# Optimization experiments

Measured on AMD Instinct MI355X. Metric: run time of the kernel, lower is better.

The kernel has to match this reference:

```python
import jax, jax.numpy as jnp
import numpy as np

B, N, E, C, M = 4, 16384, 65536, 256, 64

def setup_inputs() -> dict:
    key = jax.random.key(0)
    ks = jax.random.split(key, 12)
    s = 1.0 / np.sqrt(C)
    return {
        'x': jax.random.normal(ks[0], (B, N, C), jnp.float32),
        'edge_attr': jax.random.normal(ks[1], (B, E, 1), jnp.float32),
        'edge_idx': jax.random.randint(ks[2], (B, E, 2), 0, N, jnp.int32),
        'W_fx': jax.random.normal(ks[3], (C, C), jnp.float32) * s,
        'b_fx': jnp.zeros((C,), jnp.float32),
        'W_x': jax.random.normal(ks[4], (C, C), jnp.float32) * s,
        'b_x': jnp.zeros((C,), jnp.float32),
        'W_slice': jax.random.normal(ks[5], (C, M), jnp.float32) * s,
        'b_slice': jnp.zeros((M,), jnp.float32),
        'temp_x': jnp.full((1, 1, M), 0.5, jnp.float32),
        'ph_x': jax.random.uniform(ks[6], (1, 1, C), jnp.float32) / C,
        'W_fedge': jax.random.normal(ks[7], (1, C), jnp.float32),
        'b_fedge': jnp.zeros((C,), jnp.float32),
        'temp_edge': jnp.full((1, 1, M), 0.5, jnp.float32),
        'W_eslice': jax.random.normal(ks[8], (M, M), jnp.float32) * (1.0 / np.sqrt(M)),
        'b_eslice': jnp.zeros((M,), jnp.float32),
        'ph_edge': jax.random.uniform(ks[9], (1, 1, C), jnp.float32) / C,
    }


def reference(x, edge_attr, edge_idx, W_fx, b_fx, W_x, b_x, W_slice, b_slice,
              temp_x, ph_x, W_fedge, b_fedge, temp_edge, W_eslice, b_eslice, ph_edge):
    # node path
    fx_mid = x @ W_fx + b_fx                                  # [B,N,C]
    x_mid = x @ W_x + b_x + ph_x                              # [B,N,C]
    logits = (x_mid @ W_slice + b_slice) / jnp.clip(temp_x, 0.01, 5.0)
    slice_weight = jax.nn.softmax(logits, axis=-1)            # [B,N,M]
    slice_norm = slice_weight.sum(axis=-2)[..., None]         # [B,M,1]
    slice_token = jnp.einsum('bnm,bnc->bmc', slice_weight, fx_mid)
    # edge path
    fedge_mid = edge_attr @ W_fedge + b_fedge + ph_edge       # [B,E,C]
    gather = jax.vmap(lambda sw, idx: sw[idx])                # per-batch node gather
    sw_sum = gather(slice_weight, edge_idx[:, :, 0]) + gather(slice_weight, edge_idx[:, :, 1])
    e_logits = (sw_sum / jnp.clip(temp_edge, 0.01, 5.0)) @ W_eslice + b_eslice
    edge_slice_weight = jax.nn.softmax(e_logits, axis=-1)     # [B,E,M]
    edge_slice_norm = edge_slice_weight.sum(axis=-2)[..., None]
    edge_slice_token = jnp.einsum('bnm,bnc->bmc', edge_slice_weight, fedge_mid)
    scale = x.shape[1] / edge_attr.shape[1]
    slice_token = slice_token + edge_slice_token * scale
    slice_norm = slice_norm + edge_slice_norm * scale
    slice_token = slice_token / (slice_norm + 1e-5)
    return (slice_token, slice_weight)
```

## Files before the change

kernel.cpp:

```cpp
#include <hip/hip_runtime.h>

#define BB 4
#define NN 16384
#define EE 65536
#define CC 256
#define MM 64

#define WS_NORM   0
#define WS_T1     256
#define WS_ESN    512
#define WS_BCOMB  768
#define WS_ITX    832
#define WS_ITE    896
#define WS_WES2   1024
#define WS_WCOMB  5120
#define WS_WES2T  13312
#define WS_SW2    21504
#define WS_SSUM   WS_SW2
#define WS_SPART  4215808

typedef __attribute__((ext_vector_type(8))) __bf16 bf16x8_t;
typedef __attribute__((ext_vector_type(4))) float f32x4_t;

static __device__ __forceinline__ unsigned short f2bf(float f) {
    unsigned int u = __float_as_uint(f);
    unsigned int r = (u + 0x7FFFu + ((u >> 16) & 1u)) >> 16;
    return (unsigned short)r;
}
static __device__ __forceinline__ float bf2f(unsigned short h) {
    return __uint_as_float((unsigned int)h << 16);
}
static __device__ __forceinline__ unsigned int pk2(float a, float b) {
    return (unsigned int)f2bf(a) | ((unsigned int)f2bf(b) << 16);
}

__global__ __launch_bounds__(256) void kPP(const float* __restrict__ Wx,
                                           const float* __restrict__ Wsl,
                                           const float* __restrict__ bx,
                                           const float* __restrict__ phx,
                                           const float* __restrict__ bsl,
                                           const float* __restrict__ tx,
                                           const float* __restrict__ te,
                                           const float* __restrict__ Wes,
                                           float* __restrict__ ws) {
    __shared__ float row[256];
    __shared__ float part[4][64];
    const int tid = threadIdx.x;
    const int m = tid & 63, kq = tid >> 6;
    if (blockIdx.x < 256) {
        const int c = blockIdx.x;
        row[tid] = Wx[c * CC + tid];
        __syncthreads();
        float acc = 0.f;
#pragma unroll 8
        for (int kk = 0; kk < 64; ++kk) {
            int k = kq * 64 + kk;
            acc += row[k] * Wsl[k * MM + m];
        }
        part[kq][m] = acc;
        __syncthreads();
        if (tid < 64) {
            float v = part[0][tid] + part[1][tid] + part[2][tid] + part[3][tid];
            ((unsigned short*)(ws + WS_WCOMB))[tid * 256 + c] = f2bf(v);
        }
    } else {
#pragma unroll
        for (int i = 0; i < 3; ++i) ws[i * 256 + tid] = 0.f;
        row[tid] = bx[tid] + phx[tid];
        __syncthreads();
        float acc = 0.f;
#pragma unroll 8
        for (int kk = 0; kk < 64; ++kk) {
            int k = kq * 64 + kk;
            acc += row[k] * Wsl[k * MM + m];
        }
        part[kq][m] = acc;
        __syncthreads();
        if (tid < 64) {
            ws[WS_BCOMB + tid] = bsl[tid] +
                part[0][tid] + part[1][tid] + part[2][tid] + part[3][tid];
            ws[WS_ITX + tid] = 1.f / fminf(fmaxf(tx[tid], 0.01f), 5.f);
            ws[WS_ITE + tid] = 1.f / fminf(fmaxf(te[tid], 0.01f), 5.f);
        }
        unsigned short* w2t = (unsigned short*)(ws + WS_WES2T);
#pragma unroll
        for (int i = 0; i < 16; ++i) {
            int e = i * 256 + tid;
            int m2 = e >> 6, k2 = e & 63;
            float itk = 1.f / fminf(fmaxf(te[k2], 0.01f), 5.f);
            w2t[m2 * 64 + k2] = f2bf(itk * Wes[k2 * 64 + m2]);
        }
    }
}

#define N1_STEP(CQ, Q0, Q1)                                                     \
    {                                                                           \
        bf16x8_t bfr_[4];                                                       \
        _Pragma("unroll")                                                       \
        for (int mt = 0; mt < 4; ++mt)                                          \
            bfr_[mt] = *(const bf16x8_t*)&smem_u[(mt * 16 + ln) * 264 + (CQ) + kg * 8]; \
        union { unsigned short u[8]; bf16x8_t v; } af_;                         \
        af_.u[0]=f2bf(Q0.x); af_.u[1]=f2bf(Q0.y); af_.u[2]=f2bf(Q0.z); af_.u[3]=f2bf(Q0.w); \
        af_.u[4]=f2bf(Q1.x); af_.u[5]=f2bf(Q1.y); af_.u[6]=f2bf(Q1.z); af_.u[7]=f2bf(Q1.w); \
        _Pragma("unroll")                                                       \
        for (int mt = 0; mt < 4; ++mt)                                          \
            acc[mt] = __builtin_amdgcn_mfma_f32_16x16x32_bf16(af_.v, bfr_[mt], acc[mt], 0, 0, 0); \
    }

__global__ __launch_bounds__(256, 4) void kN1(const float* __restrict__ x,
                                              const float* __restrict__ ws,
                                              float* __restrict__ out1,
                                              unsigned short* __restrict__ sw2b,
                                              float* __restrict__ norm_acc) {
    __shared__ float smem[9472];
    __shared__ float redn[4][64];
    __shared__ float bcs[64], itxs[64];
    unsigned short* smem_u = (unsigned short*)smem;
    float* swl = smem + 2560;
    const int tid = threadIdx.x;
    const int wv = tid >> 6, l = tid & 63;
    const int ln = l & 15, kg = l >> 4;
    const int row0 = blockIdx.x * 64;
    const int b = blockIdx.x >> 8;
    const int r = tid >> 2;
    const int h = tid & 3;

    if (tid < 64) { bcs[tid] = ws[WS_BCOMB + tid]; itxs[tid] = ws[WS_ITX + tid]; }

    const unsigned short* wct = (const unsigned short*)(ws + WS_WCOMB);
#pragma unroll
    for (int i = 0; i < 8; ++i) {
        int f8 = (i * 256 + tid) * 8;
        int m = f8 >> 8, k = f8 & 255;
        *(uint4*)&smem_u[m * 264 + k] = *(const uint4*)&wct[f8];
    }
    __syncthreads();

    f32x4_t acc[4];
#pragma unroll
    for (int j = 0; j < 4; ++j) acc[j] = (f32x4_t){0.f, 0.f, 0.f, 0.f};

    const float* bp0 = x + (size_t)(row0 + wv * 16 + ln) * CC + kg * 8;
    float4 A0 = *(const float4*)(bp0), A1 = *(const float4*)(bp0 + 4);
    for (int c0 = 0; c0 < CC; c0 += 64) {
        float4 B0 = *(const float4*)(bp0 + c0 + 32), B1 = *(const float4*)(bp0 + c0 + 36);
        N1_STEP(c0, A0, A1);
        if (c0 + 64 < CC) {
            A0 = *(const float4*)(bp0 + c0 + 64); A1 = *(const float4*)(bp0 + c0 + 68);
        }
        N1_STEP(c0 + 32, B0, B1);
    }
    __syncthreads();

#pragma unroll
    for (int mt = 0; mt < 4; ++mt)
#pragma unroll
        for (int j = 0; j < 4; ++j)
            swl[(wv * 16 + kg * 4 + j) * 68 + mt * 16 + ln] = acc[mt][j];
    {
        const unsigned short* w2tg = (const unsigned short*)(ws + WS_WES2T);
        int m2 = tid >> 2, k2 = (tid & 3) * 16;
        *(uint4*)&smem_u[m2 * 80 + k2] = *(const uint4*)&w2tg[m2 * 64 + k2];
        *(uint4*)&smem_u[m2 * 80 + k2 + 8] = *(const uint4*)&w2tg[m2 * 64 + k2 + 8];
    }
    __syncthreads();

    float sacc[16];
#pragma unroll
    for (int q = 0; q < 4; ++q) {
        float4 v = *(float4*)&swl[r * 68 + h * 16 + q * 4];
        sacc[q * 4 + 0] = v.x; sacc[q * 4 + 1] = v.y;
        sacc[q * 4 + 2] = v.z; sacc[q * 4 + 3] = v.w;
    }
    float colsum[16];
    {
        float mx = -1e30f;
#pragma unroll
        for (int j = 0; j < 16; ++j) {
            int m = h * 16 + j;
            sacc[j] = (sacc[j] + bcs[m]) * itxs[m];
            mx = fmaxf(mx, sacc[j]);
        }
        mx = fmaxf(mx, __shfl_xor(mx, 1));
        mx = fmaxf(mx, __shfl_xor(mx, 2));
        float s = 0.f;
#pragma unroll
        for (int j = 0; j < 16; ++j) { sacc[j] = __expf(sacc[j] - mx); s += sacc[j]; }
        s += __shfl_xor(s, 1);
        s += __shfl_xor(s, 2);
        float inv = 1.f / s;
        int row = row0 + r;
#pragma unroll
        for (int q = 0; q < 4; ++q) {
            float4 v = {sacc[q * 4 + 0] * inv, sacc[q * 4 + 1] * inv,
                        sacc[q * 4 + 2] * inv, sacc[q * 4 + 3] * inv};
            *(float4*)(out1 + (size_t)row * MM + h * 16 + q * 4) = v;
            *(float4*)&swl[r * 68 + h * 16 + q * 4] = v;
            colsum[q * 4 + 0] = v.x; colsum[q * 4 + 1] = v.y;
            colsum[q * 4 + 2] = v.z; colsum[q * 4 + 3] = v.w;
        }
    }
#pragma unroll
    for (int j = 0; j < 16; ++j) {
        colsum[j] += __shfl_xor(colsum[j], 4);
        colsum[j] += __shfl_xor(colsum[j], 8);
        colsum[j] += __shfl_xor(colsum[j], 16);
        colsum[j] += __shfl_xor(colsum[j], 32);
    }
    if (l < 4) {
#pragma unroll
        for (int j = 0; j < 16; ++j) redn[wv][h * 16 + j] = colsum[j];
    }
    __syncthreads();

    f32x4_t eacc[4];
#pragma unroll
    for (int j = 0; j < 4; ++j) eacc[j] = (f32x4_t){0.f, 0.f, 0.f, 0.f};
#pragma unroll
    for (int ks = 0; ks < 2; ++ks) {
        bf16x8_t bfw[4];
#pragma unroll
        for (int mt = 0; mt < 4; ++mt)
            bfw[mt] = *(const bf16x8_t*)&smem_u[(mt * 16 + ln) * 80 + ks * 32 + kg * 8];
        const float* ap = &swl[(wv * 16 + ln) * 68 + ks * 32 + kg * 8];
        float4 p0 = *(const float4*)ap;
        float4 p1 = *(const float4*)(ap + 4);
        union { unsigned short u[8]; bf16x8_t v; } af;
        af.u[0] = f2bf(p0.x); af.u[1] = f2bf(p0.y);
        af.u[2] = f2bf(p0.z); af.u[3] = f2bf(p0.w);
        af.u[4] = f2bf(p1.x); af.u[5] = f2bf(p1.y);
        af.u[6] = f2bf(p1.z); af.u[7] = f2bf(p1.w);
#pragma unroll
        for (int mt = 0; mt < 4; ++mt)
            eacc[mt] = __builtin_amdgcn_mfma_f32_16x16x32_bf16(
                af.v, bfw[mt], eacc[mt], 0, 0, 0);
    }
    {
        unsigned short* esb = (unsigned short*)(smem + 6912);
#pragma unroll
        for (int mt = 0; mt < 4; ++mt)
#pragma unroll
            for (int j = 0; j < 4; ++j)
                esb[(wv * 16 + kg * 4 + j) * 80 + mt * 16 + ln] = f2bf(eacc[mt][j]);
    }
    __syncthreads();
    {
        const unsigned short* esb = (const unsigned short*)(smem + 6912);
        int row = tid >> 2, q = tid & 3;
        const uint4* src = (const uint4*)&esb[row * 80 + q * 16];
        uint4* dst = (uint4*)(sw2b + (size_t)(row0 + row) * MM + q * 16);
        dst[0] = src[0]; dst[1] = src[1];
    }

    if (tid < 64)
        atomicAdd(&norm_acc[b * MM + tid],
                  redn[0][tid] + redn[1][tid] + redn[2][tid] + redn[3][tid]);
}

__global__ __launch_bounds__(256, 4) void kEN2(const float* __restrict__ x,
                                               const float* __restrict__ sw,
                                               float* __restrict__ Spart,
                                               int PB, int rowsPB, int nb2,
                                               const float* __restrict__ eattr,
                                               const int* __restrict__ eidx,
                                               const unsigned short* __restrict__ sw2b,
                                               const float* __restrict__ bes,
                                               float* __restrict__ t1_acc,
                                               float* __restrict__ esn_acc) {
    __shared__ float smem[5184];
    const int tid = threadIdx.x;
    if ((int)blockIdx.x < nb2) {
        unsigned short* xT = (unsigned short*)smem;
        unsigned short* sT = (unsigned short*)(smem + 2560);
        const int bid = blockIdx.x;
        const int ch = bid & 1;
        const int p = (bid >> 1) % PB, b = (bid >> 1) / PB;
        const int base = b * NN + p * rowsPB;
        const int wv = tid >> 6, l = tid & 63;
        const int ln = l & 15, kg = l >> 4;
        const int ct0 = wv * 2;

        f32x4_t acc[2][4];
#pragma unroll
        for (int i = 0; i < 2; ++i)
#pragma unroll
            for (int j = 0; j < 4; ++j) acc[i][j] = (f32x4_t){0.f, 0.f, 0.f, 0.f};

        for (int r0 = 0; r0 < rowsPB; r0 += 32) {
            __syncthreads();
#pragma unroll
            for (int i = 0; i < 2; ++i) {
                int task = i * 256 + tid;
                int rp = task >> 5;
                int cq = (task & 31) * 4;
                int ra = 2 * rp;
                const float* xa = x + (size_t)(base + r0 + ra) * CC + ch * 128 + cq;
                float4 va = *(const float4*)xa;
                float4 vb = *(const float4*)(xa + CC);
                int key = (cq >> 2) & 3;
                int off = ((ra >> 3) ^ key) * 8 + (ra & 7);
                *(unsigned int*)&xT[(cq + 0) * 40 + off] = pk2(va.x, vb.x);
                *(unsigned int*)&xT[(cq + 1) * 40 + off] = pk2(va.y, vb.y);
                *(unsigned int*)&xT[(cq + 2) * 40 + off] = pk2(va.z, vb.z);
                *(unsigned int*)&xT[(cq + 3) * 40 + off] = pk2(va.w, vb.w);
            }
            {
                int rp = tid >> 4, mq = (tid & 15) * 4;
                int ra = 2 * rp;
                const float* sa = sw + (size_t)(base + r0 + ra) * MM + mq;
                float4 va = *(const float4*)sa;
                float4 vb = *(const float4*)(sa + MM);
                int key = (mq >> 2) & 3;
                int off = ((ra >> 3) ^ key) * 8 + (ra & 7);
                *(unsigned int*)&sT[(mq + 0) * 40 + off] = pk2(va.x, vb.x);
                *(unsigned int*)&sT[(mq + 1) * 40 + off] = pk2(va.y, vb.y);
                *(unsigned int*)&sT[(mq + 2) * 40 + off] = pk2(va.z, vb.z);
                *(unsigned int*)&sT[(mq + 3) * 40 + off] = pk2(va.w, vb.w);
            }
            __syncthreads();
            bf16x8_t afr[4];
#pragma unroll
            for (int mt = 0; mt < 4; ++mt) {
                int m = mt * 16 + ln;
                int chunk = kg ^ ((m >> 2) & 3);
                afr[mt] = *(const bf16x8_t*)&sT[m * 40 + chunk * 8];
            }
#pragma unroll
            for (int ct = 0; ct < 2; ++ct) {
                int c = (ct0 + ct) * 16 + ln;
                int chunk = kg ^ ((c >> 2) & 3);
                bf16x8_t bfr = *(const bf16x8_t*)&xT[c * 40 + chunk * 8];
#pragma unroll
                for (int mt = 0; mt < 4; ++mt)
                    acc[ct][mt] = __builtin_amdgcn_mfma_f32_16x16x32_bf16(
                        afr[mt], bfr, acc[ct][mt], 0, 0, 0);
            }
        }
        float* dst = Spart + (size_t)(b * PB + p) * MM * CC + ch * 128;
#pragma unroll
        for (int ct = 0; ct < 2; ++ct)
#pragma unroll
            for (int mt = 0; mt < 4; ++mt)
#pragma unroll
                for (int j = 0; j < 4; ++j) {
                    int m = mt * 16 + kg * 4 + j;
                    int c = (ct0 + ct) * 16 + ln;
                    dst[(size_t)m * CC + c] = acc[ct][mt][j];
                }
    } else {
        unsigned short* uu = (unsigned short*)smem;
        float* eav  = smem + 4352;
        float* redt = smem + 4608;
        float* redn = smem + 4864;
        float* bes_s = smem + 5120;
        const int w = tid >> 6, l = tid & 63;
        const int eg = ((int)blockIdx.x - nb2) * 256 + tid;
        const int b = eg >> 16;
        if (tid < 64) bes_s[tid] = bes[tid];
        const int2 idx = ((const int2*)eidx)[eg];
        const float ea = eattr[eg];
        const uint4* g0 = (const uint4*)(sw2b + (size_t)(b * NN + idx.x) * MM);
        const uint4* g1 = (const uint4*)(sw2b + (size_t)(b * NN + idx.y) * MM);
        eav[w * 64 + l] = ea;
        __syncthreads();

        float v[64];
#pragma unroll
        for (int q = 0; q < 8; ++q) {
            uint4 a = g0[q], c = g1[q];
            unsigned int au[4] = {a.x, a.y, a.z, a.w};
            unsigned int cu[4] = {c.x, c.y, c.z, c.w};
#pragma unroll
            for (int j = 0; j < 4; ++j) {
                int m = q * 8 + j * 2;
                v[m + 0] = __uint_as_float(au[j] << 16) + __uint_as_float(cu[j] << 16) + bes_s[m + 0];
                v[m + 1] = __uint_as_float(au[j] & 0xFFFF0000u) + __uint_as_float(cu[j] & 0xFFFF0000u) + bes_s[m + 1];
            }
        }
        float mx = -1e30f;
#pragma unroll
        for (int m = 0; m < 64; ++m) mx = fmaxf(mx, v[m]);
        float s = 0.f;
#pragma unroll
        for (int m = 0; m < 64; ++m) { v[m] = __expf(v[m] - mx); s += v[m]; }
        float inv = 1.f / s;

        const int ml = l & 31, rh = l >> 5;
#pragma unroll
        for (int ph = 0; ph < 2; ++ph) {
            __syncthreads();
#pragma unroll
            for (int j = 0; j < 32; j += 2)
                *(unsigned int*)&uu[w * 2176 + l * 34 + j] =
                    pk2(v[ph * 32 + j] * inv, v[ph * 32 + j + 1] * inv);
            __syncthreads();
            float t = 0.f, n = 0.f;
#pragma unroll 8
            for (int rr = 0; rr < 32; ++rr) {
                int r = rh * 32 + rr;
                float e = bf2f(uu[w * 2176 + r * 34 + ml]);
                n += e;
                t += e * eav[w * 64 + r];
            }
            t += __shfl_xor(t, 32);
            n += __shfl_xor(n, 32);
            if (l < 32) { redt[w * 64 + ph * 32 + l] = t; redn[w * 64 + ph * 32 + l] = n; }
        }
        __syncthreads();
        if (tid < 64) {
            atomicAdd(&t1_acc[b * 64 + tid],
                      redt[tid] + redt[64 + tid] + redt[128 + tid] + redt[192 + tid]);
            atomicAdd(&esn_acc[b * 64 + tid],
                      redn[tid] + redn[64 + tid] + redn[128 + tid] + redn[192 + tid]);
        }
    }
}

__global__ __launch_bounds__(256) void kR(const float* __restrict__ Spart,
                                          float* __restrict__ Ssum, int PB) {
    const int idx = blockIdx.x * 256 + threadIdx.x;
    const int b = idx >> 14;
    const int mc = idx & 16383;
    const float* sp = Spart + (size_t)b * PB * MM * CC + mc;
    float a0 = 0.f, a1 = 0.f, a2 = 0.f, a3 = 0.f;
    for (int p = 0; p < PB; p += 4) {
        a0 += sp[(size_t)(p + 0) * MM * CC];
        a1 += sp[(size_t)(p + 1) * MM * CC];
        a2 += sp[(size_t)(p + 2) * MM * CC];
        a3 += sp[(size_t)(p + 3) * MM * CC];
    }
    Ssum[idx] = (a0 + a1) + (a2 + a3);
}

__global__ __launch_bounds__(256) void kF2(const float* __restrict__ ws,
                                           const float* __restrict__ Wfx,
                                           const float* __restrict__ bfx,
                                           const float* __restrict__ Wfe,
                                           const float* __restrict__ bfe,
                                           const float* __restrict__ phe,
                                           float* __restrict__ out0) {
    __shared__ float srow[256];
    const int bid = blockIdx.x;
    const int b = bid >> 6, m = bid & 63;
    const int t = threadIdx.x;
    srow[t] = ws[WS_SSUM + (size_t)(b * MM + m) * CC + t];
    __syncthreads();
    float acc = 0.f;
#pragma unroll 8
    for (int k = 0; k < 256; ++k) acc += srow[k] * Wfx[k * CC + t];
    float nv  = ws[WS_NORM + b * 64 + m];
    float t1v = ws[WS_T1   + b * 64 + m];
    float ev  = ws[WS_ESN  + b * 64 + m];
    const float scale = (float)NN / (float)EE;
    float num = acc + nv * bfx[t] + scale * (t1v * Wfe[t] + ev * (bfe[t] + phe[t]));
    float den = nv + scale * ev + 1e-5f;
    out0[(size_t)(b * MM + m) * CC + t] = num / den;
}

extern "C" void kernel_launch(void* const* d_in, const int* in_sizes, int n_in,
                              void* d_out, int out_size, void* d_ws, size_t ws_size,
                              hipStream_t stream) {
    const float* x     = (const float*)d_in[0];
    const float* eattr = (const float*)d_in[1];
    const int*   eidx  = (const int*)d_in[2];
    const float* Wfx   = (const float*)d_in[3];
    const float* bfx   = (const float*)d_in[4];
    const float* Wx    = (const float*)d_in[5];
    const float* bx    = (const float*)d_in[6];
    const float* Wsl   = (const float*)d_in[7];
    const float* bsl   = (const float*)d_in[8];
    const float* tx    = (const float*)d_in[9];
    const float* phx   = (const float*)d_in[10];
    const float* Wfe   = (const float*)d_in[11];
    const float* bfe   = (const float*)d_in[12];
    const float* te    = (const float*)d_in[13];
    const float* Wes   = (const float*)d_in[14];
    const float* bes   = (const float*)d_in[15];
    const float* phe   = (const float*)d_in[16];

    float* out0 = (float*)d_out;
    float* out1 = out0 + (size_t)BB * MM * CC;
    float* ws   = (float*)d_ws;
    unsigned short* sw2b = (unsigned short*)(ws + WS_SW2);

    int PB = 32;
    while (PB > 8) {
        size_t need = (size_t)(WS_SPART + (size_t)BB * PB * MM * CC) * sizeof(float);
        if (need <= ws_size) break;
        PB >>= 1;
    }
    int rowsPB = NN / PB;
    int nb2 = BB * PB * 2;

    kPP<<<257, 256, 0, stream>>>(Wx, Wsl, bx, phx, bsl, tx, te, Wes, ws);
    kN1<<<1024, 256, 0, stream>>>(x, ws, out1, sw2b, ws + WS_NORM);
    kEN2<<<nb2 + EE * BB / 256, 256, 0, stream>>>(x, out1, ws + WS_SPART, PB, rowsPB, nb2,
                                                  eattr, eidx, sw2b, bes,
                                                  ws + WS_T1, ws + WS_ESN);
    kR <<<1024, 256, 0, stream>>>(ws + WS_SPART, ws + WS_SSUM, PB);
    kF2<<<256, 256, 0, stream>>>(ws, Wfx, bfx, Wfe, bfe, phe, out0);
}
```

Measured before the change: 92.55 us.

## Fuse slice-token GEMM into node kernel with atomic accumulation, drop partial-sum reduce

The slice_weight^T·x GEMM moves out of the edge kernel's extra blocks and into kN1. Each node block reuses its own softmax weights from registers and re-reads its 64-row x tile into swizzled LDS, then atomically adds its 64x256 contribution into a zeroed Ssum buffer (zeroed in kPP). This removes the separate reduce kernel kR and the large partial-sum workspace traffic, and the edge kernel now launches only edge blocks. In exchange kN1 uses more shared memory and a lower occupancy bound, and it issues many float atomics per block (1024 blocks × 16K atomics), which may contend and makes the summation order nondeterministic.

Measured after the change: 127.0 us. 1.37x slower.

```diff
diff --git a/kernel.cpp b/kernel.cpp
--- a/kernel.cpp
+++ b/kernel.cpp
@@ -16,8 +16,7 @@
 #define WS_WCOMB  5120
 #define WS_WES2T  13312
 #define WS_SW2    21504
-#define WS_SSUM   WS_SW2
-#define WS_SPART  4215808
+#define WS_SSUM   4215808
 
 typedef __attribute__((ext_vector_type(8))) __bf16 bf16x8_t;
 typedef __attribute__((ext_vector_type(4))) float f32x4_t;
@@ -48,6 +47,8 @@
     const int tid = threadIdx.x;
     const int m = tid & 63, kq = tid >> 6;
     if (blockIdx.x < 256) {
+        float4 z = {0.f, 0.f, 0.f, 0.f};
+        *(float4*)&ws[WS_SSUM + blockIdx.x * 1024 + tid * 4] = z;
         const int c = blockIdx.x;
         row[tid] = Wx[c * CC + tid];
         __syncthreads();
@@ -107,12 +108,13 @@
             acc[mt] = __builtin_amdgcn_mfma_f32_16x16x32_bf16(af_.v, bfr_[mt], acc[mt], 0, 0, 0); \
     }
 
-__global__ __launch_bounds__(256, 4) void kN1(const float* __restrict__ x,
+__global__ __launch_bounds__(256, 3) void kN1(const float* __restrict__ x,
                                               const float* __restrict__ ws,
                                               float* __restrict__ out1,
                                               unsigned short* __restrict__ sw2b,
+                                              float* __restrict__ ssum,
                                               float* __restrict__ norm_acc) {
-    __shared__ float smem[9472];
+    __shared__ float smem[11520];
     __shared__ float redn[4][64];
     __shared__ float bcs[64], itxs[64];
     unsigned short* smem_u = (unsigned short*)smem;
@@ -191,9 +193,11 @@
         float inv = 1.f / s;
         int row = row0 + r;
 #pragma unroll
+        for (int j = 0; j < 16; ++j) sacc[j] *= inv;
+#pragma unroll
         for (int q = 0; q < 4; ++q) {
-            float4 v = {sacc[q * 4 + 0] * inv, sacc[q * 4 + 1] * inv,
-                        sacc[q * 4 + 2] * inv, sacc[q * 4 + 3] * inv};
+            float4 v = {sacc[q * 4 + 0], sacc[q * 4 + 1],
+                        sacc[q * 4 + 2], sacc[q * 4 + 3]};
             *(float4*)(out1 + (size_t)row * MM + h * 16 + q * 4) = v;
             *(float4*)&swl[r * 68 + h * 16 + q * 4] = v;
             colsum[q * 4 + 0] = v.x; colsum[q * 4 + 1] = v.y;
@@ -213,29 +217,29 @@
     }
     __syncthreads();
 
-    f32x4_t eacc[4];
-#pragma unroll
-    for (int j = 0; j < 4; ++j) eacc[j] = (f32x4_t){0.f, 0.f, 0.f, 0.f};
-#pragma unroll
-    for (int ks = 0; ks < 2; ++ks) {
-        bf16x8_t bfw[4];
-#pragma unroll
-        for (int mt = 0; mt < 4; ++mt)
-            bfw[mt] = *(const bf16x8_t*)&smem_u[(mt * 16 + ln) * 80 + ks * 32 + kg * 8];
-        const float* ap = &swl[(wv * 16 + ln) * 68 + ks * 32 + kg * 8];
-        float4 p0 = *(const float4*)ap;
-        float4 p1 = *(const float4*)(ap + 4);
-        union { unsigned short u[8]; bf16x8_t v; } af;
-        af.u[0] = f2bf(p0.x); af.u[1] = f2bf(p0.y);
-        af.u[2] = f2bf(p0.z); af.u[3] = f2bf(p0.w);
-        af.u[4] = f2bf(p1.x); af.u[5] = f2bf(p1.y);
-        af.u[6] = f2bf(p1.z); af.u[7] = f2bf(p1.w);
-#pragma unroll
-        for (int mt = 0; mt < 4; ++mt)
-            eacc[mt] = __builtin_amdgcn_mfma_f32_16x16x32_bf16(
-                af.v, bfw[mt], eacc[mt], 0, 0, 0);
-    }
-    {
+    {
+        f32x4_t eacc[4];
+#pragma unroll
+        for (int j = 0; j < 4; ++j) eacc[j] = (f32x4_t){0.f, 0.f, 0.f, 0.f};
+#pragma unroll
+        for (int ks = 0; ks < 2; ++ks) {
+            bf16x8_t bfw[4];
+#pragma unroll
+            for (int mt = 0; mt < 4; ++mt)
+                bfw[mt] = *(const bf16x8_t*)&smem_u[(mt * 16 + ln) * 80 + ks * 32 + kg * 8];
+            const float* ap = &swl[(wv * 16 + ln) * 68 + ks * 32 + kg * 8];
+            float4 p0 = *(const float4*)ap;
+            float4 p1 = *(const float4*)(ap + 4);
+            union { unsigned short u[8]; bf16x8_t v; } af;
+            af.u[0] = f2bf(p0.x); af.u[1] = f2bf(p0.y);
+            af.u[2] = f2bf(p0.z); af.u[3] = f2bf(p0.w);
+            af.u[4] = f2bf(p1.x); af.u[5] = f2bf(p1.y);
+            af.u[6] = f2bf(p1.z); af.u[7] = f2bf(p1.w);
+#pragma unroll
+            for (int mt = 0; mt < 4; ++mt)
+                eacc[mt] = __builtin_amdgcn_mfma_f32_16x16x32_bf16(
+                    af.v, bfw[mt], eacc[mt], 0, 0, 0);
+        }
         unsigned short* esb = (unsigned short*)(smem + 6912);
 #pragma unroll
         for (int mt = 0; mt < 4; ++mt)
@@ -251,10 +255,81 @@
         uint4* dst = (uint4*)(sw2b + (size_t)(row0 + row) * MM + q * 16);
         dst[0] = src[0]; dst[1] = src[1];
     }
-
     if (tid < 64)
         atomicAdd(&norm_acc[b * MM + tid],
                   redn[0][tid] + redn[1][tid] + redn[2][tid] + redn[3][tid]);
+    __syncthreads();
+
+    {
+        unsigned short* xT  = smem_u;
+        unsigned short* sT  = (unsigned short*)(smem + 9216);
+#pragma unroll
+        for (int j = 0; j < 16; ++j) {
+            int m = h * 16 + j;
+            int key = (m >> 2) & 3;
+            int off = (r >> 5) * 32 + (((r & 31) >> 3) ^ key) * 8 + (r & 7);
+            sT[m * 72 + off] = f2bf(sacc[j]);
+        }
+#pragma unroll
+        for (int i = 0; i < 8; ++i) {
+            int task = i * 256 + tid;
+            int rp = task >> 6;
+            int cq = (task & 63) * 4;
+            int ra = 2 * rp;
+            const float* xa = x + (size_t)(row0 + ra) * CC + cq;
+            float4 va = *(const float4*)xa;
+            float4 vb = *(const float4*)(xa + CC);
+#pragma unroll
+            for (int t = 0; t < 4; ++t) {
+                int c = cq + t;
+                int key = (c >> 2) & 3;
+                int off = (ra >> 5) * 32 + (((ra & 31) >> 3) ^ key) * 8 + (ra & 7);
+                float av = (t == 0) ? va.x : (t == 1) ? va.y : (t == 2) ? va.z : va.w;
+                float bvv = (t == 0) ? vb.x : (t == 1) ? vb.y : (t == 2) ? vb.z : vb.w;
+                *(unsigned int*)&xT[c * 72 + off] = pk2(av, bvv);
+            }
+        }
+        __syncthreads();
+        float* sdst = ssum + (size_t)b * MM * CC;
+#pragma unroll
+        for (int ctg = 0; ctg < 2; ++ctg) {
+            f32x4_t sa[2][4];
+#pragma unroll
+            for (int i = 0; i < 2; ++i)
+#pragma unroll
+                for (int j = 0; j < 4; ++j) sa[i][j] = (f32x4_t){0.f, 0.f, 0.f, 0.f};
+#pragma unroll
+            for (int ks = 0; ks < 2; ++ks) {
+                bf16x8_t afr[4];
+#pragma unroll
+                for (int mt = 0; mt < 4; ++mt) {
+                    int m = mt * 16 + ln;
+                    int chunk = kg ^ ((m >> 2) & 3);
+                    afr[mt] = *(const bf16x8_t*)&sT[m * 72 + ks * 32 + chunk * 8];
+                }
+#pragma unroll
+                for (int ct = 0; ct < 2; ++ct) {
+                    int c = (wv * 4 + ctg * 2 + ct) * 16 + ln;
+                    int chunk = kg ^ ((c >> 2) & 3);
+                    bf16x8_t bfr = *(const bf16x8_t*)&xT[c * 72 + ks * 32 + chunk * 8];
+#pragma unroll
+                    for (int mt = 0; mt < 4; ++mt)
+                        sa[ct][mt] = __builtin_amdgcn_mfma_f32_16x16x32_bf16(
+                            afr[mt], bfr, sa[ct][mt], 0, 0, 0);
+                }
+            }
+#pragma unroll
+            for (int ct = 0; ct < 2; ++ct)
+#pragma unroll
+                for (int mt = 0; mt < 4; ++mt)
+#pragma unroll
+                    for (int j = 0; j < 4; ++j) {
+                        int m = mt * 16 + kg * 4 + j;
+                        int c = (wv * 4 + ctg * 2 + ct) * 16 + ln;
+                        atomicAdd(&sdst[(size_t)m * CC + c], sa[ct][mt][j]);
+                    }
+        }
+    }
 }
 
 __global__ __launch_bounds__(256, 4) void kEN2(const float* __restrict__ x,
@@ -269,92 +344,14 @@
                                                float* __restrict__ esn_acc) {
     __shared__ float smem[5184];
     const int tid = threadIdx.x;
-    if ((int)blockIdx.x < nb2) {
-        unsigned short* xT = (unsigned short*)smem;
-        unsigned short* sT = (unsigned short*)(smem + 2560);
-        const int bid = blockIdx.x;
-        const int ch = bid & 1;
-        const int p = (bid >> 1) % PB, b = (bid >> 1) / PB;
-        const int base = b * NN + p * rowsPB;
-        const int wv = tid >> 6, l = tid & 63;
-        const int ln = l & 15, kg = l >> 4;
-        const int ct0 = wv * 2;
-
-        f32x4_t acc[2][4];
-#pragma unroll
-        for (int i = 0; i < 2; ++i)
-#pragma unroll
-            for (int j = 0; j < 4; ++j) acc[i][j] = (f32x4_t){0.f, 0.f, 0.f, 0.f};
-
-        for (int r0 = 0; r0 < rowsPB; r0 += 32) {
-            __syncthreads();
-#pragma unroll
-            for (int i = 0; i < 2; ++i) {
-                int task = i * 256 + tid;
-                int rp = task >> 5;
-                int cq = (task & 31) * 4;
-                int ra = 2 * rp;
-                const float* xa = x + (size_t)(base + r0 + ra) * CC + ch * 128 + cq;
-                float4 va = *(const float4*)xa;
-                float4 vb = *(const float4*)(xa + CC);
-                int key = (cq >> 2) & 3;
-                int off = ((ra >> 3) ^ key) * 8 + (ra & 7);
-                *(unsigned int*)&xT[(cq + 0) * 40 + off] = pk2(va.x, vb.x);
-                *(unsigned int*)&xT[(cq + 1) * 40 + off] = pk2(va.y, vb.y);
-                *(unsigned int*)&xT[(cq + 2) * 40 + off] = pk2(va.z, vb.z);
-                *(unsigned int*)&xT[(cq + 3) * 40 + off] = pk2(va.w, vb.w);
-            }
-            {
-                int rp = tid >> 4, mq = (tid & 15) * 4;
-                int ra = 2 * rp;
-                const float* sa = sw + (size_t)(base + r0 + ra) * MM + mq;
-                float4 va = *(const float4*)sa;
-                float4 vb = *(const float4*)(sa + MM);
-                int key = (mq >> 2) & 3;
-                int off = ((ra >> 3) ^ key) * 8 + (ra & 7);
-                *(unsigned int*)&sT[(mq + 0) * 40 + off] = pk2(va.x, vb.x);
-                *(unsigned int*)&sT[(mq + 1) * 40 + off] = pk2(va.y, vb.y);
-                *(unsigned int*)&sT[(mq + 2) * 40 + off] = pk2(va.z, vb.z);
-                *(unsigned int*)&sT[(mq + 3) * 40 + off] = pk2(va.w, vb.w);
-            }
-            __syncthreads();
-            bf16x8_t afr[4];
-#pragma unroll
-            for (int mt = 0; mt < 4; ++mt) {
-                int m = mt * 16 + ln;
-                int chunk = kg ^ ((m >> 2) & 3);
-                afr[mt] = *(const bf16x8_t*)&sT[m * 40 + chunk * 8];
-            }
-#pragma unroll
-            for (int ct = 0; ct < 2; ++ct) {
-                int c = (ct0 + ct) * 16 + ln;
-                int chunk = kg ^ ((c >> 2) & 3);
-                bf16x8_t bfr = *(const bf16x8_t*)&xT[c * 40 + chunk * 8];
-#pragma unroll
-                for (int mt = 0; mt < 4; ++mt)
-                    acc[ct][mt] = __builtin_amdgcn_mfma_f32_16x16x32_bf16(
-                        afr[mt], bfr, acc[ct][mt], 0, 0, 0);
-            }
-        }
-        float* dst = Spart + (size_t)(b * PB + p) * MM * CC + ch * 128;
-#pragma unroll
-        for (int ct = 0; ct < 2; ++ct)
-#pragma unroll
-            for (int mt = 0; mt < 4; ++mt)
-#pragma unroll
-                for (int j = 0; j < 4; ++j) {
-                    int m = mt * 16 + kg * 4 + j;
-                    int c = (ct0 + ct) * 16 + ln;
-                    dst[(size_t)m * CC + c] = acc[ct][mt][j];
-                }
-    } else {
+    {
         unsigned short* uu = (unsigned short*)smem;
         float* eav  = smem + 4352;
         float* redt = smem + 4608;
         float* redn = smem + 4864;
         float* bes_s = smem + 5120;
         const int w = tid >> 6, l = tid & 63;
-        const int eg = ((int)blockIdx.x - nb2) * 256 + tid;
+        const int eg = (int)blockIdx.x * 256 + tid;
         const int b = eg >> 16;
         if (tid < 64) bes_s[tid] = bes[tid];
         const int2 idx = ((const int2*)eidx)[eg];
@@ -414,22 +411,6 @@
                       redn[tid] + redn[64 + tid] + redn[128 + tid] + redn[192 + tid]);
         }
     }
-}
-
-__global__ __launch_bounds__(256) void kR(const float* __restrict__ Spart,
-                                          float* __restrict__ Ssum, int PB) {
-    const int idx = blockIdx.x * 256 + threadIdx.x;
-    const int b = idx >> 14;
-    const int mc = idx & 16383;
-    const float* sp = Spart + (size_t)b * PB * MM * CC + mc;
-    float a0 = 0.f, a1 = 0.f, a2 = 0.f, a3 = 0.f;
-    for (int p = 0; p < PB; p += 4) {
-        a0 += sp[(size_t)(p + 0) * MM * CC];
-        a1 += sp[(size_t)(p + 1) * MM * CC];
-        a2 += sp[(size_t)(p + 2) * MM * CC];
-        a3 += sp[(size_t)(p + 3) * MM * CC];
-    }
-    Ssum[idx] = (a0 + a1) + (a2 + a3);
 }
 
 __global__ __launch_bounds__(256) void kF2(const float* __restrict__ ws,
@@ -483,20 +464,10 @@
     float* ws   = (float*)d_ws;
     unsigned short* sw2b = (unsigned short*)(ws + WS_SW2);
 
-    int PB = 32;
-    while (PB > 8) {
-        size_t need = (size_t)(WS_SPART + (size_t)BB * PB * MM * CC) * sizeof(float);
-        if (need <= ws_size) break;
-        PB >>= 1;
-    }
-    int rowsPB = NN / PB;
-    int nb2 = BB * PB * 2;
-
     kPP<<<257, 256, 0, stream>>>(Wx, Wsl, bx, phx, bsl, tx, te, Wes, ws);
-    kN1<<<1024, 256, 0, stream>>>(x, ws, out1, sw2b, ws + WS_NORM);
-    kEN2<<<nb2 + EE * BB / 256, 256, 0, stream>>>(x, out1, ws + WS_SPART, PB, rowsPB, nb2,
-                                                  eattr, eidx, sw2b, bes,
-                                                  ws + WS_T1, ws + WS_ESN);
-    kR <<<1024, 256, 0, stream>>>(ws + WS_SPART, ws + WS_SSUM, PB);
+    kN1<<<1024, 256, 0, stream>>>(x, ws, out1, sw2b, ws + WS_SSUM, ws + WS_NORM);
+    kEN2<<<EE * BB / 256, 256, 0, stream>>>(x, out1, nullptr, 0, 0, 0,
+                                            eattr, eidx, sw2b, bes,
+                                            ws + WS_T1, ws + WS_ESN);
     kF2<<<256, 256, 0, stream>>>(ws, Wfx, bfx, Wfe, bfe, phe, out0);
 }
```
